# Kernel tuning notes

Measured on AMD Instinct MI355X. Metric: run time of the kernel, lower is better.

The kernel has to match this reference:

```python
import jax, jax.numpy as jnp
import numpy as np

NUM_CLASSES = 41


def conv3x3(x, w):
    # x: [B,Cin,H,W], w: [Cout,Cin,3,3], padding=1, bias=False
    return jax.lax.conv_general_dilated(
        x, w, window_strides=(1, 1), padding=((1, 1), (1, 1)),
        dimension_numbers=("NCHW", "OIHW", "NCHW"))


def ra_module(feats, labels_ds, w1, w2, key):
    """RA: per-(batch,label) segment-mean of features, replacing the
    original nested python loops with one fused segment_sum.
    feats: [b,c,h,w]; labels_ds: [b,h,w] int; w1: [c//16,c]; w2: [c,c//16]."""
    b, c, h, w = feats.shape
    n = h * w
    f = feats.reshape(b, c, n).transpose(0, 2, 1).reshape(b * n, c)  # [b*n, c]
    seg = (jnp.arange(b, dtype=jnp.int32)[:, None] * NUM_CLASSES
           + labels_ds.reshape(b, n)).reshape(-1)                    # [b*n]
    sums = jax.ops.segment_sum(f, seg, num_segments=b * NUM_CLASSES)
    cnt = jax.ops.segment_sum(jnp.ones((b * n,), f.dtype), seg,
                              num_segments=b * NUM_CLASSES)
    mean = sums / jnp.maximum(cnt, 1.0)[:, None]
    # torch code initializes the queue with randn and only overwrites
    # classes present in the label map; absent classes keep random values.
    init = jax.random.normal(key, (b * NUM_CLASSES, c), dtype=f.dtype)
    queue = jnp.where((cnt > 0)[:, None], mean, init).reshape(b, NUM_CLASSES, c)
    # F.normalize(att, dim=1): L2-normalize across the class dimension
    att = queue / jnp.maximum(
        jnp.linalg.norm(queue, axis=1, keepdims=True), 1e-12)
    att = att.sum(axis=1)                                            # [b, c]
    hid = jax.nn.relu(att @ w1.T)                                    # 1x1 conv on 1x1 map == matmul
    out = jax.nn.sigmoid(hid @ w2.T)                                 # [b, c]
    return out[:, :, None, None]


def setup_inputs() -> dict:
    key = jax.random.key(0)
    ks = jax.random.split(key, 8)
    B, C, H, W = 4, 128, 224, 224
    r = jax.random.normal(ks[0], (B, C, H, W), dtype=jnp.float32)
    d = jax.random.normal(ks[1], (B, C, H, W), dtype=jnp.float32)
    label = jax.random.randint(ks[2], (B, 4 * H, 4 * W), 0, NUM_CLASSES,
                               dtype=jnp.int32)
    w_fuse = jax.random.normal(ks[3], (C, 2 * C, 3, 3), dtype=jnp.float32) * 0.02
    w1_d = jax.random.normal(ks[4], (C // 16, C), dtype=jnp.float32) * 0.1
    w2_d = jax.random.normal(ks[5], (C, C // 16), dtype=jnp.float32) * 0.1
    w1_f = jax.random.normal(ks[6], (C // 16, C), dtype=jnp.float32) * 0.1
    w2_f = jax.random.normal(ks[7], (C, C // 16), dtype=jnp.float32) * 0.1
    return {"r": r, "d": d, "label": label, "w_fuse": w_fuse,
            "w1_d": w1_d, "w2_d": w2_d, "w1_f": w1_f, "w2_f": w2_f}


def reference(r, d, label, w_fuse, w1_d, w2_d, w1_f, w2_f):
    # nearest-neighbor downsample of labels to feature resolution
    # (exact integer ratio 4 -> strided slice, matches torch 'nearest')
    labels_ds = label[:, ::4, ::4]
    add = r + d
    mul = r * jax.nn.sigmoid(d)
    fuse = conv3x3(jnp.concatenate([add, mul], axis=1), w_fuse)
    d_ra = d * ra_module(d, labels_ds, w1_d, w2_d, jax.random.key(1))
    fuse_ra = fuse * ra_module(fuse, labels_ds, w1_f, w2_f, jax.random.key(2))
    return fuse_ra + d_ra
```

## Files before the change

### kernel.cpp

```cpp
#include <hip/hip_runtime.h>
#include <hip/hip_bf16.h>
#include <cstdint>
#include <cstddef>

typedef unsigned short u16;
typedef unsigned int   u32;
typedef unsigned char  u8;

#define NCLS 41

typedef short s16x8 __attribute__((ext_vector_type(8)));
typedef float f32x4 __attribute__((ext_vector_type(4)));

__device__ __forceinline__ u16 f2bf(float f) {
  u32 u = __float_as_uint(f);
  u += 0x7fffu + ((u >> 16) & 1u);
  return (u16)(u >> 16);
}

#if __has_builtin(__builtin_amdgcn_global_load_lds)
#define HAVE_GLL 1
typedef const __attribute__((address_space(1))) u32* gas1p;
typedef __attribute__((address_space(3))) u32* las3p;
__device__ __forceinline__ void gll16(const void* g, void* l) {
  __builtin_amdgcn_global_load_lds((gas1p)g, (las3p)l, 16, 0, 0);
}
#else
#define HAVE_GLL 0
#endif

__global__ void k_wprep(const float* __restrict__ wf, u16* __restrict__ Wt) {
  const int e = blockIdx.x * 256 + threadIdx.x;
  if (e >= 9 * 128 * 256) return;
  const int tap = e / (128 * 256);
  const int oc  = (e / 256) % 128;
  const int ic  = e % 256;
  Wt[e] = f2bf(wf[((size_t)oc * 256 + ic) * 9 + tap]);
}

__global__ void k_labels(const int* __restrict__ label, u8* __restrict__ labs,
                         int* __restrict__ counts) {
  const int i = blockIdx.x % 224, b = blockIdx.x / 224;
  __shared__ int hist[NCLS];
  const int t = threadIdx.x;
  if (t < NCLS) hist[t] = 0;
  __syncthreads();
  if (t < 224) {
    const int v = label[((size_t)b * 896 + 4 * i) * 896 + 4 * t];
    labs[((size_t)b * 224 + i) * 224 + t] = (u8)v;
    atomicAdd(&hist[v], 1);
  }
  __syncthreads();
  if (t < NCLS) atomicAdd(&counts[b * NCLS + t], hist[t]);
}

__global__ __launch_bounds__(256) void k_prep(const float* __restrict__ r,
                                              const float* __restrict__ d,
                                              const u8* __restrict__ labs,
                                              u16* __restrict__ X,
                                              float* __restrict__ sums_d) {
  const int t  = threadIdx.x;
  const int g  = blockIdx.x & 1;
  const int yp = (blockIdx.x >> 1) % 226;
  const int b  = blockIdx.x / 452;

  if (yp == 0 || yp == 225) {
    for (int e = t; e < 4 * 226 * 4; e += 256) {
      const int sl = e / 904, rm = e % 904;
      const int s = (sl & 1) + g * 2 + (sl >> 1) * 4;
      uint4* p = (uint4*)(X + (((size_t)(b * 226 + yp) * 8 + s) * 226) * 32) + rm;
      *p = uint4{0u, 0u, 0u, 0u};
    }
    return;
  }
  const int y = yp - 1;

  __shared__ float acc[NCLS * 65];
  for (int e = t; e < NCLS * 65; e += 256) acc[e] = 0.f;
  __syncthreads();

  if (t < 224) {
    const int x = t;
    const int lab = (int)labs[((size_t)b * 224 + y) * 224 + x];
    const float* rb = r + ((size_t)b * 128 + g * 64) * 50176 + y * 224 + x;
    const float* db = d + ((size_t)b * 128 + g * 64) * 50176 + y * 224 + x;
    for (int c0 = 0; c0 < 64; c0 += 16) {
      float rv[16], dv[16];
#pragma unroll
      for (int j = 0; j < 16; ++j) {
        rv[j] = rb[(size_t)(c0 + j) * 50176];
        dv[j] = db[(size_t)(c0 + j) * 50176];
      }
#pragma unroll
      for (int j = 0; j < 16; ++j)
        atomicAdd(&acc[lab * 65 + c0 + j], dv[j]);
      u32 pa[8], pm[8];
#pragma unroll
      for (int j = 0; j < 8; ++j) {
        const float r0 = rv[2 * j], r1 = rv[2 * j + 1];
        const float d0 = dv[2 * j], d1 = dv[2 * j + 1];
        pa[j] = (u32)f2bf(r0 + d0) | ((u32)f2bf(r1 + d1) << 16);
        pm[j] = (u32)f2bf(r0 / (1.f + __expf(-d0)))
              | ((u32)f2bf(r1 / (1.f + __expf(-d1))) << 16);
      }
      const int s  = g * 2 + (c0 >> 5);
      const int qo = (c0 & 31) >> 1;
      u32* Xa = (u32*)(X + ((((size_t)(b * 226 + yp) * 8 + s)     * 226) + (x + 1)) * 32) + qo;
      u32* Xm = (u32*)(X + ((((size_t)(b * 226 + yp) * 8 + s + 4) * 226) + (x + 1)) * 32) + qo;
      *(uint4*)(Xa)     = uint4{pa[0], pa[1], pa[2], pa[3]};
      *(uint4*)(Xa + 4) = uint4{pa[4], pa[5], pa[6], pa[7]};
      *(uint4*)(Xm)     = uint4{pm[0], pm[1], pm[2], pm[3]};
      *(uint4*)(Xm + 4) = uint4{pm[4], pm[5], pm[6], pm[7]};
    }
  } else {
    const int idx = t - 224;
    const int chunk = idx & 3, pxsel = (idx >> 2) & 1, sl = idx >> 3;
    const int s = (sl & 1) + g * 2 + (sl >> 1) * 4;
    const int px = pxsel * 225;
    uint4* p = (uint4*)(X + ((((size_t)(b * 226 + yp) * 8 + s) * 226) + px) * 32) + chunk;
    *p = uint4{0u, 0u, 0u, 0u};
  }
  __syncthreads();
  for (int e = t; e < NCLS * 64; e += 256)
    atomicAdd(&sums_d[(size_t)b * NCLS * 128 + (e >> 6) * 128 + g * 64 + (e & 63)],
              acc[(e >> 6) * 65 + (e & 63)]);
}

__global__ __launch_bounds__(256) void k_conv(const u16* __restrict__ X,
                                              const u16* __restrict__ Wt,
                                              u16* __restrict__ fuse) {
  __shared__ u16 Alds[128 * 32];
  __shared__ u16 Blds[128 * 32];
  const int t = threadIdx.x;
  const int w = t >> 6, l = t & 63;
  const int lrow = l & 15, lq = l >> 4;
  const int wm = (w & 1) * 64, wn = (w >> 1) * 64;

  const int L   = blockIdx.x;
  const int xcd = L & 7;
  const int i   = L >> 3;
  const int b   = i / 56;
  const int rem = i % 56;
  const int y   = xcd * 28 + (rem >> 1);
  const int x0  = (rem & 1) * 128;

  f32x4 acc[4][4] = {};

  const int posA = t >> 2;
  const int koff = (t & 3) * 8;
  char* ldsA0 = (char*)Alds + (w * 64) * 16;
  char* ldsB0 = (char*)Blds + (w * 64) * 16;

  for (int tap = 0; tap < 9; ++tap) {
    const int dy = tap / 3, dx = tap % 3;
    const size_t rowb = (size_t)(b * 226 + y + dy) * 8;
    const u16* Bbase = Wt + (size_t)tap * (128 * 256);
    for (int s = 0; s < 8; ++s) {
      const u16* ga0 = X + ((rowb + s) * 226 + (x0 + dx) + posA) * 32 + koff;
      const u16* gb0 = Bbase + (size_t)posA * 256 + s * 32 + koff;
#if HAVE_GLL
      gll16(ga0, ldsA0);
      gll16(gb0, ldsB0);
      gll16(ga0 + 64 * 32,  ldsA0 + 256 * 16);
      gll16(gb0 + 64 * 256, ldsB0 + 256 * 16);
#else
      *(uint4*)((char*)Alds + (size_t)t * 16)         = *(const uint4*)ga0;
      *(uint4*)((char*)Blds + (size_t)t * 16)         = *(const uint4*)gb0;
      *(uint4*)((char*)Alds + (size_t)(256 + t) * 16) = *(const uint4*)(ga0 + 64 * 32);
      *(uint4*)((char*)Blds + (size_t)(256 + t) * 16) = *(const uint4*)(gb0 + 64 * 256);
#endif
      __syncthreads();
      s16x8 af[4], bfr[4];
#pragma unroll
      for (int mi = 0; mi < 4; ++mi)
        af[mi] = *(const s16x8*)((const char*)Alds + (wm + mi * 16 + lrow) * 64 + lq * 16);
#pragma unroll
      for (int ni = 0; ni < 4; ++ni)
        bfr[ni] = *(const s16x8*)((const char*)Blds + (wn + ni * 16 + lrow) * 64 + lq * 16);
#pragma unroll
      for (int mi = 0; mi < 4; ++mi)
#pragma unroll
        for (int ni = 0; ni < 4; ++ni)
          acc[mi][ni] = __builtin_amdgcn_mfma_f32_16x16x32_bf16(af[mi], bfr[ni], acc[mi][ni], 0, 0, 0);
      __syncthreads();
    }
  }
#pragma unroll
  for (int mi = 0; mi < 4; ++mi) {
#pragma unroll
    for (int rr = 0; rr < 4; ++rr) {
      const int pos = wm + mi * 16 + lq * 4 + rr;
      const int x = x0 + pos;
      if (x < 224) {
        u16* dst = fuse + ((size_t)(b * 224 + y) * 224 + x) * 128;
#pragma unroll
        for (int ni = 0; ni < 4; ++ni) {
          const int oc = wn + ni * 16 + lrow;
          dst[oc] = f2bf(acc[mi][ni][rr]);
        }
      }
    }
  }
}

__global__ __launch_bounds__(256) void k_segf(const u16* __restrict__ fuse,
                                              const u8* __restrict__ labs,
                                              float* __restrict__ sums_f) {
  const int y = blockIdx.x % 224, b = blockIdx.x / 224;
  __shared__ float acc[NCLS * 129];
  __shared__ u8 ll[224];
  const int t = threadIdx.x;
  for (int e = t; e < NCLS * 129; e += 256) acc[e] = 0.f;
  if (t < 224) ll[t] = labs[((size_t)b * 224 + y) * 224 + t];
  __syncthreads();
  const u32* fb = (const u32*)(fuse + ((size_t)b * 224 + y) * 224 * 128);
  for (int e = t; e < 224 * 64; e += 256) {
    const int c2 = e % 64, px = e / 64;
    const u32 v = fb[(size_t)px * 64 + c2];
    const int lab = ll[px];
    atomicAdd(&acc[lab * 129 + 2 * c2],     __uint_as_float(v << 16));
    atomicAdd(&acc[lab * 129 + 2 * c2 + 1], __uint_as_float(v & 0xffff0000u));
  }
  __syncthreads();
  for (int e = t; e < NCLS * 128; e += 256)
    atomicAdd(&sums_f[b * NCLS * 128 + e], acc[(e / 128) * 129 + (e % 128)]);
}

__global__ __launch_bounds__(256) void k_gates(const float* __restrict__ sums,
                                               const int* __restrict__ counts,
                                               const float* __restrict__ w1,
                                               const float* __restrict__ w2,
                                               float* __restrict__ gates) {
  const int b = blockIdx.x;
  __shared__ float att[128];
  __shared__ float hid[8];
  const int t = threadIdx.x;
  if (t < 128) {
    float s1 = 0.f, s2 = 0.f;
    for (int lb = 0; lb < NCLS; ++lb) {
      const float cnt = (float)counts[b * NCLS + lb];
      const float m = sums[(size_t)b * NCLS * 128 + lb * 128 + t] / fmaxf(cnt, 1.f);
      s1 += m; s2 += m * m;
    }
    att[t] = s1 / fmaxf(sqrtf(s2), 1e-12f);
  }
  __syncthreads();
  if (t < 8) {
    float h = 0.f;
    for (int c = 0; c < 128; ++c) h += att[c] * w1[t * 128 + c];
    hid[t] = fmaxf(h, 0.f);
  }
  __syncthreads();
  if (t < 128) {
    float o = 0.f;
    for (int j = 0; j < 8; ++j) o += hid[j] * w2[t * 8 + j];
    gates[b * 128 + t] = 1.f / (1.f + expf(-o));
  }
}

__global__ __launch_bounds__(256) void k_out(const u16* __restrict__ fuse,
                                             const float* __restrict__ d,
                                             const float* __restrict__ gates,
                                             float* __restrict__ out) {
  const int y = blockIdx.x % 224, b = blockIdx.x / 224;
  __shared__ float flds[224 * 33];
  __shared__ float gf[128], gd[128];
  const int t = threadIdx.x;
  if (t < 128) gd[t] = gates[b * 128 + t];
  else         gf[t - 128] = gates[512 + b * 128 + (t - 128)];
  const u32* frow = (const u32*)fuse + ((size_t)b * 224 + y) * 224 * 64;
  const float* db = d + (size_t)b * 128 * 50176 + y * 224;
  float* ob = out + (size_t)b * 128 * 50176 + y * 224;
  for (int c0 = 0; c0 < 128; c0 += 32) {
    __syncthreads();
    for (int e = t; e < 224 * 16; e += 256) {
      const int px = e / 16, q = e % 16;
      const u32 v = frow[(size_t)px * 64 + (c0 >> 1) + q];
      flds[px * 33 + 2 * q]     = __uint_as_float(v << 16);
      flds[px * 33 + 2 * q + 1] = __uint_as_float(v & 0xffff0000u);
    }
    __syncthreads();
    for (int e = t; e < 32 * 224; e += 256) {
      const int cc = e / 224, x = e % 224, c = c0 + cc;
      ob[(size_t)c * 50176 + x] = flds[x * 33 + cc] * gf[c] + db[(size_t)c * 50176 + x] * gd[c];
    }
  }
}

extern "C" void kernel_launch(void* const* d_in, const int* in_sizes, int n_in,
                              void* d_out, int out_size, void* d_ws, size_t ws_size,
                              hipStream_t stream) {
  const float* r     = (const float*)d_in[0];
  const float* d     = (const float*)d_in[1];
  const int*   label = (const int*)d_in[2];
  const float* wf    = (const float*)d_in[3];
  const float* w1d   = (const float*)d_in[4];
  const float* w2d   = (const float*)d_in[5];
  const float* w1f   = (const float*)d_in[6];
  const float* w2f   = (const float*)d_in[7];
  float* out = (float*)d_out;

  char* ws = (char*)d_ws;
  size_t off = 0;
  auto carve = [&](size_t bytes) -> char* {
    char* p = ws + off;
    off = (off + bytes + 511) & ~(size_t)511;
    return p;
  };
  u16* X       = (u16*)carve((size_t)4 * 226 * 226 * 256 * 2 + 65536);
  u16* Wt      = (u16*)carve((size_t)9 * 128 * 256 * 2);
  u16* fuseb   = (u16*)carve((size_t)4 * 224 * 224 * 128 * 2);
  u8*  labs    = (u8*) carve((size_t)4 * 224 * 224);
  int* counts  = (int*)carve(4 * NCLS * sizeof(int));
  float* sumsd = (float*)carve((size_t)4 * NCLS * 128 * 4);
  float* sumsf = (float*)carve((size_t)4 * NCLS * 128 * 4);
  float* gates = (float*)carve(1024 * sizeof(float));

  hipMemsetAsync(counts, 0, 4 * NCLS * sizeof(int), stream);
  hipMemsetAsync(sumsd, 0, (size_t)4 * NCLS * 128 * 4, stream);
  hipMemsetAsync(sumsf, 0, (size_t)4 * NCLS * 128 * 4, stream);
  k_wprep <<<(9 * 128 * 256 + 255) / 256, 256, 0, stream>>>(wf, Wt);
  k_labels<<<4 * 224, 256, 0, stream>>>(label, labs, counts);
  k_prep  <<<4 * 226 * 2, 256, 0, stream>>>(r, d, labs, X, sumsd);
  k_conv  <<<1792, 256, 0, stream>>>(X, Wt, fuseb);
  k_segf  <<<4 * 224, 256, 0, stream>>>(fuseb, labs, sumsf);
  k_gates <<<4, 256, 0, stream>>>(sumsd, counts, w1d, w2d, gates);
  k_gates <<<4, 256, 0, stream>>>(sumsf, counts, w1f, w2f, gates + 512);
  k_out   <<<4 * 224, 256, 0, stream>>>(fuseb, d, gates, out);
}
```

Before: 753.0 us.

## Double-buffer conv LDS tiles to overlap global loads with MFMA compute

```diff
diff --git a/kernel.cpp b/kernel.cpp
--- a/kernel.cpp
+++ b/kernel.cpp
@@ -129,8 +129,8 @@
 __global__ __launch_bounds__(256) void k_conv(const u16* __restrict__ X,
                                               const u16* __restrict__ Wt,
                                               u16* __restrict__ fuse) {
-  __shared__ u16 Alds[128 * 32];
-  __shared__ u16 Blds[128 * 32];
+  __shared__ u16 Alds[2][128 * 32];
+  __shared__ u16 Blds[2][128 * 32];
   const int t = threadIdx.x;
   const int w = t >> 6, l = t & 63;
   const int lrow = l & 15, lq = l >> 4;
@@ -148,42 +148,50 @@
 
   const int posA = t >> 2;
   const int koff = (t & 3) * 8;
-  char* ldsA0 = (char*)Alds + (w * 64) * 16;
-  char* ldsB0 = (char*)Blds + (w * 64) * 16;
-
-  for (int tap = 0; tap < 9; ++tap) {
+  const size_t browb = (size_t)(b * 226 + y) * 8;
+  const int ldsoff = (w * 64) * 16;
+
+  auto stage = [&](int step, int buf) {
+    const int tap = step >> 3, s = step & 7;
     const int dy = tap / 3, dx = tap % 3;
-    const size_t rowb = (size_t)(b * 226 + y + dy) * 8;
-    const u16* Bbase = Wt + (size_t)tap * (128 * 256);
-    for (int s = 0; s < 8; ++s) {
-      const u16* ga0 = X + ((rowb + s) * 226 + (x0 + dx) + posA) * 32 + koff;
-      const u16* gb0 = Bbase + (size_t)posA * 256 + s * 32 + koff;
+    const u16* ga0 = X + ((browb + dy * 8 + s) * 226 + (x0 + dx) + posA) * 32 + koff;
+    const u16* gb0 = Wt + (size_t)tap * (128 * 256) + (size_t)posA * 256 + s * 32 + koff;
+    char* la = (char*)Alds[buf] + ldsoff;
+    char* lb = (char*)Blds[buf] + ldsoff;
 #if HAVE_GLL
-      gll16(ga0, ldsA0);
-      gll16(gb0, ldsB0);
-      gll16(ga0 + 64 * 32,  ldsA0 + 256 * 16);
-      gll16(gb0 + 64 * 256, ldsB0 + 256 * 16);
+    gll16(ga0, la);
+    gll16(gb0, lb);
+    gll16(ga0 + 64 * 32,  la + 256 * 16);
+    gll16(gb0 + 64 * 256, lb + 256 * 16);
 #else
-      *(uint4*)((char*)Alds + (size_t)t * 16)         = *(const uint4*)ga0;
-      *(uint4*)((char*)Blds + (size_t)t * 16)         = *(const uint4*)gb0;
-      *(uint4*)((char*)Alds + (size_t)(256 + t) * 16) = *(const uint4*)(ga0 + 64 * 32);
-      *(uint4*)((char*)Blds + (size_t)(256 + t) * 16) = *(const uint4*)(gb0 + 64 * 256);
+    *(uint4*)((char*)Alds[buf] + (size_t)t * 16)         = *(const uint4*)ga0;
+    *(uint4*)((char*)Blds[buf] + (size_t)t * 16)         = *(const uint4*)gb0;
+    *(uint4*)((char*)Alds[buf] + (size_t)(256 + t) * 16) = *(const uint4*)(ga0 + 64 * 32);
+    *(uint4*)((char*)Blds[buf] + (size_t)(256 + t) * 16) = *(const uint4*)(gb0 + 64 * 256);
 #endif
-      __syncthreads();
-      s16x8 af[4], bfr[4];
-#pragma unroll
-      for (int mi = 0; mi < 4; ++mi)
-        af[mi] = *(const s16x8*)((const char*)Alds + (wm + mi * 16 + lrow) * 64 + lq * 16);
+  };
+
+  stage(0, 0);
+  __syncthreads();
+  int cur = 0;
+  for (int step = 0; step < 72; ++step) {
+    if (step < 71) stage(step + 1, cur ^ 1);
+    const char* A = (const char*)Alds[cur];
+    const char* B = (const char*)Blds[cur];
+    s16x8 af[4], bfr[4];
+#pragma unroll
+    for (int mi = 0; mi < 4; ++mi)
+      af[mi] = *(const s16x8*)(A + (wm + mi * 16 + lrow) * 64 + lq * 16);
+#pragma unroll
+    for (int ni = 0; ni < 4; ++ni)
+      bfr[ni] = *(const s16x8*)(B + (wn + ni * 16 + lrow) * 64 + lq * 16);
+#pragma unroll
+    for (int mi = 0; mi < 4; ++mi)
 #pragma unroll
       for (int ni = 0; ni < 4; ++ni)
-        bfr[ni] = *(const s16x8*)((const char*)Blds + (wn + ni * 16 + lrow) * 64 + lq * 16);
-#pragma unroll
-      for (int mi = 0; mi < 4; ++mi)
-#pragma unroll
-        for (int ni = 0; ni < 4; ++ni)
-          acc[mi][ni] = __builtin_amdgcn_mfma_f32_16x16x32_bf16(af[mi], bfr[ni], acc[mi][ni], 0, 0, 0);
-      __syncthreads();
-    }
+        acc[mi][ni] = __builtin_amdgcn_mfma_f32_16x16x32_bf16(af[mi], bfr[ni], acc[mi][ni], 0, 0, 0);
+    __syncthreads();
+    cur ^= 1;
   }
 #pragma unroll
   for (int mi = 0; mi < 4; ++mi) {
```

After: 786.9 us. 4.5% more time.

## Reuse one input row tile across the three horizontal conv taps

Applied to the files above, without the earlier changes.

```diff
diff --git a/kernel.cpp b/kernel.cpp
--- a/kernel.cpp
+++ b/kernel.cpp
@@ -129,8 +129,8 @@
 __global__ __launch_bounds__(256) void k_conv(const u16* __restrict__ X,
                                               const u16* __restrict__ Wt,
                                               u16* __restrict__ fuse) {
-  __shared__ u16 Alds[128 * 32];
-  __shared__ u16 Blds[128 * 32];
+  __shared__ u16 Alds[132 * 32];
+  __shared__ u16 Blds[3][128 * 32];
   const int t = threadIdx.x;
   const int w = t >> 6, l = t & 63;
   const int lrow = l & 15, lq = l >> 4;
@@ -148,40 +148,49 @@
 
   const int posA = t >> 2;
   const int koff = (t & 3) * 8;
+  const size_t browb = (size_t)(b * 226 + y) * 8;
   char* ldsA0 = (char*)Alds + (w * 64) * 16;
-  char* ldsB0 = (char*)Blds + (w * 64) * 16;
-
-  for (int tap = 0; tap < 9; ++tap) {
-    const int dy = tap / 3, dx = tap % 3;
-    const size_t rowb = (size_t)(b * 226 + y + dy) * 8;
-    const u16* Bbase = Wt + (size_t)tap * (128 * 256);
+
+  for (int dy = 0; dy < 3; ++dy) {
     for (int s = 0; s < 8; ++s) {
-      const u16* ga0 = X + ((rowb + s) * 226 + (x0 + dx) + posA) * 32 + koff;
-      const u16* gb0 = Bbase + (size_t)posA * 256 + s * 32 + koff;
+      const u16* Abase = X + ((browb + dy * 8 + s) * 226 + x0) * 32;
 #if HAVE_GLL
-      gll16(ga0, ldsA0);
-      gll16(gb0, ldsB0);
-      gll16(ga0 + 64 * 32,  ldsA0 + 256 * 16);
-      gll16(gb0 + 64 * 256, ldsB0 + 256 * 16);
+      gll16(Abase + posA * 32 + koff,        ldsA0);
+      gll16(Abase + (64 + posA) * 32 + koff, ldsA0 + 4096);
 #else
-      *(uint4*)((char*)Alds + (size_t)t * 16)         = *(const uint4*)ga0;
-      *(uint4*)((char*)Blds + (size_t)t * 16)         = *(const uint4*)gb0;
-      *(uint4*)((char*)Alds + (size_t)(256 + t) * 16) = *(const uint4*)(ga0 + 64 * 32);
-      *(uint4*)((char*)Blds + (size_t)(256 + t) * 16) = *(const uint4*)(gb0 + 64 * 256);
+      *(uint4*)((char*)Alds + t * 16)        = *(const uint4*)(Abase + posA * 32 + koff);
+      *(uint4*)((char*)Alds + 4096 + t * 16) = *(const uint4*)(Abase + (64 + posA) * 32 + koff);
 #endif
+      if (t < 8)
+        *(uint4*)((char*)Alds + 8192 + t * 16) = *(const uint4*)(Abase + 128 * 32 + t * 8);
+#pragma unroll
+      for (int dx = 0; dx < 3; ++dx) {
+        const u16* Bbase = Wt + (size_t)(dy * 3 + dx) * (128 * 256) + s * 32;
+        char* ldsB0 = (char*)Blds[dx] + (w * 64) * 16;
+#if HAVE_GLL
+        gll16(Bbase + posA * 256 + koff,        ldsB0);
+        gll16(Bbase + (64 + posA) * 256 + koff, ldsB0 + 4096);
+#else
+        *(uint4*)((char*)Blds[dx] + t * 16)        = *(const uint4*)(Bbase + posA * 256 + koff);
+        *(uint4*)((char*)Blds[dx] + 4096 + t * 16) = *(const uint4*)(Bbase + (64 + posA) * 256 + koff);
+#endif
+      }
       __syncthreads();
-      s16x8 af[4], bfr[4];
-#pragma unroll
-      for (int mi = 0; mi < 4; ++mi)
-        af[mi] = *(const s16x8*)((const char*)Alds + (wm + mi * 16 + lrow) * 64 + lq * 16);
-#pragma unroll
-      for (int ni = 0; ni < 4; ++ni)
-        bfr[ni] = *(const s16x8*)((const char*)Blds + (wn + ni * 16 + lrow) * 64 + lq * 16);
-#pragma unroll
-      for (int mi = 0; mi < 4; ++mi)
+#pragma unroll
+      for (int dx = 0; dx < 3; ++dx) {
+        s16x8 af[4], bfr[4];
+#pragma unroll
+        for (int mi = 0; mi < 4; ++mi)
+          af[mi] = *(const s16x8*)((const char*)Alds + (wm + mi * 16 + lrow + dx) * 64 + lq * 16);
 #pragma unroll
         for (int ni = 0; ni < 4; ++ni)
-          acc[mi][ni] = __builtin_amdgcn_mfma_f32_16x16x32_bf16(af[mi], bfr[ni], acc[mi][ni], 0, 0, 0);
+          bfr[ni] = *(const s16x8*)((const char*)Blds[dx] + (wn + ni * 16 + lrow) * 64 + lq * 16);
+#pragma unroll
+        for (int mi = 0; mi < 4; ++mi)
+#pragma unroll
+          for (int ni = 0; ni < 4; ++ni)
+            acc[mi][ni] = __builtin_amdgcn_mfma_f32_16x16x32_bf16(af[mi], bfr[ni], acc[mi][ni], 0, 0, 0);
+      }
       __syncthreads();
     }
   }
```

Result: faster. 720.6 us (-4.3%).
